# Kernel tuning notes

Measured on AMD Instinct MI355X. Metric: run time of the kernel, lower is better.

## Reference

```python
import jax, jax.numpy as jnp
import numpy as np

N_NODES = 100000
N_EDGES = 600000
D_FEAT = 128          # node embedding dim; in_channels = 2*D_FEAT = 256
HIDDEN = [128, 64]
OUT = 2


def setup_inputs() -> dict:
    key = jax.random.key(0)
    ks = jax.random.split(key, 8)
    enc = jax.random.normal(ks[0], (N_NODES, D_FEAT), dtype=jnp.float32)
    edge_index = jax.random.randint(ks[1], (2, N_EDGES), 0, N_NODES, dtype=jnp.int64)
    d_in = 2 * D_FEAT
    # Linear params, (in, out) layout; kaiming-ish scale
    W1 = jax.random.normal(ks[2], (d_in, HIDDEN[0]), dtype=jnp.float32) / np.sqrt(d_in)
    b1 = jnp.zeros((HIDDEN[0],), dtype=jnp.float32)
    W2 = jax.random.normal(ks[3], (HIDDEN[0], HIDDEN[1]), dtype=jnp.float32) / np.sqrt(HIDDEN[0])
    b2 = jnp.zeros((HIDDEN[1],), dtype=jnp.float32)
    W3 = jax.random.normal(ks[4], (HIDDEN[1], OUT), dtype=jnp.float32) / np.sqrt(HIDDEN[1])
    b3 = jnp.zeros((OUT,), dtype=jnp.float32)
    return {"encoder_output": enc, "edge_index": edge_index,
            "W1": W1, "b1": b1, "W2": W2, "b2": b2, "W3": W3, "b3": b3}


def reference(encoder_output, edge_index, W1, b1, W2, b2, W3, b3):
    row, col = edge_index[0], edge_index[1]
    # gather endpoint embeddings and concat -> [E, 2*D]
    x = jnp.concatenate([encoder_output[row], encoder_output[col]], axis=-1)
    h = jax.nn.relu(x @ W1 + b1)          # [E, 128]
    h = jax.nn.relu(h @ W2 + b2)          # [E, 64]
    logits = h @ W3 + b3                  # [E, 2]
    return jax.nn.log_softmax(logits, axis=-1)
```

## Files before the change

kernel.cpp:

```cpp
#include <hip/hip_runtime.h>
#include <hip/hip_fp16.h>

#define E_TOTAL  600000
#define N_NODES  100000
#define DFEAT    128
#define TPB_TILES 2
#define EPT      128
#define EPB      (EPT * TPB_TILES)
#define NB       ((E_TOTAL + EPB - 1) / EPB)

typedef __attribute__((ext_vector_type(8))) short     short8;
typedef __attribute__((ext_vector_type(8))) _Float16  half8;
typedef __attribute__((ext_vector_type(4))) float     f32x4;

static __device__ __forceinline__ unsigned short f2h(float f) {
    _Float16 h = (_Float16)f;
    return __builtin_bit_cast(unsigned short, h);
}

static __device__ __forceinline__ f32x4 mfma_f16(short8 a, short8 b, f32x4 c) {
    return __builtin_amdgcn_mfma_f32_16x16x32_f16(
        __builtin_bit_cast(half8, a), __builtin_bit_cast(half8, b), c, 0, 0, 0);
}

static __device__ __forceinline__ short8 h8_add_relu(short8 a, short8 b) {
    half8 s = __builtin_bit_cast(half8, a) + __builtin_bit_cast(half8, b);
    half8 z = {};
    s = __builtin_elementwise_max(s, z);
    return __builtin_bit_cast(short8, s);
}

__global__ void prep_w_fast(const float* __restrict__ W1, const float* __restrict__ W2,
                            unsigned short* __restrict__ w1abt, unsigned short* __restrict__ w2t) {
    int i = blockIdx.x * blockDim.x + threadIdx.x;
    if (i < 256 * 128) {
        int c = i >> 7, k = i & 127;
        w1abt[i] = f2h(W1[(k + (c & 128)) * 128 + (c & 127)]);
    } else {
        int j = i - 256 * 128;
        if (j < 64 * 128) {
            int c = j >> 7, k = j & 127;
            w2t[j] = f2h(W2[k * 64 + c]);
        }
    }
}

__global__ __launch_bounds__(256, 4) void build_pq(
        const float* __restrict__ enc, const float* __restrict__ b1,
        const unsigned short* __restrict__ w1abt, unsigned short* __restrict__ PQ)
{
    __shared__ unsigned short sX[64 * 128];

    const int tid = threadIdx.x, lane = tid & 63, w = tid >> 6;
    const int acol = lane & 15, g = lane >> 4;
    const int n0 = blockIdx.x * 64;

    {
        int r = tid >> 2, q = tid & 3;
        int n = n0 + r; if (n >= N_NODES) n = N_NODES - 1;
        const float* src = enc + (size_t)n * DFEAT + q * 32;
#pragma unroll
        for (int i = 0; i < 4; ++i) {
            float4 v0 = *reinterpret_cast<const float4*>(src + i * 8);
            float4 v1 = *reinterpret_cast<const float4*>(src + i * 8 + 4);
            short8 pv;
            pv[0] = (short)f2h(v0.x); pv[1] = (short)f2h(v0.y);
            pv[2] = (short)f2h(v0.z); pv[3] = (short)f2h(v0.w);
            pv[4] = (short)f2h(v1.x); pv[5] = (short)f2h(v1.y);
            pv[6] = (short)f2h(v1.z); pv[7] = (short)f2h(v1.w);
            int chunk = (q * 4 + i) ^ (r & 7);
            *reinterpret_cast<short8*>(&sX[r * 128 + chunk * 8]) = pv;
        }
    }
    float b1v[4];
#pragma unroll
    for (int ni = 0; ni < 4; ++ni) {
        int c = w * 64 + ni * 16 + acol;
        b1v[ni] = (c < 128) ? b1[c] : 0.f;
    }
    __syncthreads();

    f32x4 acc[4][4];
#pragma unroll
    for (int mi = 0; mi < 4; ++mi)
#pragma unroll
        for (int ni = 0; ni < 4; ++ni)
            acc[mi][ni] = (f32x4){0.f, 0.f, 0.f, 0.f};

#pragma unroll
    for (int ks = 0; ks < 4; ++ks) {
        short8 a[4];
#pragma unroll
        for (int mi = 0; mi < 4; ++mi) {
            int r = mi * 16 + acol;
            a[mi] = *reinterpret_cast<const short8*>(&sX[r * 128 + (((ks * 4 + g) ^ (r & 7)) * 8)]);
        }
#pragma unroll
        for (int ni = 0; ni < 4; ++ni) {
            int c = w * 64 + ni * 16 + acol;
            short8 bf = *reinterpret_cast<const short8*>(w1abt + c * 128 + ks * 32 + g * 8);
#pragma unroll
            for (int mi = 0; mi < 4; ++mi)
                acc[mi][ni] = mfma_f16(a[mi], bf, acc[mi][ni]);
        }
    }

#pragma unroll
    for (int mi = 0; mi < 4; ++mi)
#pragma unroll
        for (int rr = 0; rr < 4; ++rr) {
            int n = n0 + mi * 16 + g * 4 + rr;
            if (n < N_NODES) {
                unsigned short* dst = PQ + (size_t)n * 256 + w * 64 + acol;
#pragma unroll
                for (int ni = 0; ni < 4; ++ni)
                    dst[ni * 16] = f2h(acc[mi][ni][rr] + b1v[ni]);
            }
        }
}

__global__ __launch_bounds__(512, 4) void edge_head(
        const unsigned short* __restrict__ PQ,
        const int* __restrict__ eidx,
        const unsigned short* __restrict__ w2t,
        const float* __restrict__ b2, const float* __restrict__ W3, const float* __restrict__ b3,
        float* __restrict__ out)
{
    __shared__ unsigned short sH1[128 * 128];
    __shared__ unsigned short sW2[64 * 128];
    __shared__ float sB2[64];
    __shared__ float sW3[128];

    const int tid = threadIdx.x, lane = tid & 63, w = tid >> 6;
    const int e16 = lane & 15, g = lane >> 4;
    const int le = tid >> 2, q = tid & 3;

    {
        int c = tid >> 3, s = tid & 7;
#pragma unroll
        for (int h = 0; h < 2; ++h) {
            int cs = s + h * 8;
            short8 v = *reinterpret_cast<const short8*>(w2t + c * 128 + cs * 8);
            *reinterpret_cast<short8*>(&sW2[c * 128 + ((cs ^ (c & 7)) * 8)]) = v;
        }
    }
    if (tid < 64)       sB2[tid] = b2[tid];
    else if (tid < 192) sW3[tid - 64] = W3[tid - 64];
    const float b3v0 = b3[0], b3v1 = b3[1];

    const int tile0 = blockIdx.x * TPB_TILES;
    short8 rp[4], rq[4];
    {
        int e = tile0 * EPT + le; if (e >= E_TOTAL) e = E_TOTAL - 1;
        int sn = eidx[e], dn = eidx[E_TOTAL + e];
        const unsigned short* ps = PQ + (size_t)sn * 256 + q * 32;
        const unsigned short* pd = PQ + (size_t)dn * 256 + 128 + q * 32;
#pragma unroll
        for (int i = 0; i < 4; ++i) {
            rp[i] = *reinterpret_cast<const short8*>(ps + i * 8);
            rq[i] = *reinterpret_cast<const short8*>(pd + i * 8);
        }
    }

    for (int tl = 0; tl < TPB_TILES; ++tl) {
        const int tile = tile0 + tl;

#pragma unroll
        for (int i = 0; i < 4; ++i) {
            short8 hv = h8_add_relu(rp[i], rq[i]);
            int chunk = (q * 4 + i) ^ (le & 7);
            *reinterpret_cast<short8*>(&sH1[le * 128 + chunk * 8]) = hv;
        }

        if (tl + 1 < TPB_TILES) {
            int e = (tile + 1) * EPT + le; if (e >= E_TOTAL) e = E_TOTAL - 1;
            int sn = eidx[e], dn = eidx[E_TOTAL + e];
            const unsigned short* ps = PQ + (size_t)sn * 256 + q * 32;
            const unsigned short* pd = PQ + (size_t)dn * 256 + 128 + q * 32;
#pragma unroll
            for (int i = 0; i < 4; ++i) {
                rp[i] = *reinterpret_cast<const short8*>(ps + i * 8);
                rq[i] = *reinterpret_cast<const short8*>(pd + i * 8);
            }
        }
        __syncthreads();

        const int hrow = w * 16 + e16;
        f32x4 acc[4];
#pragma unroll
        for (int t = 0; t < 4; ++t) acc[t] = (f32x4){0.f, 0.f, 0.f, 0.f};
#pragma unroll
        for (int ks = 0; ks < 4; ++ks) {
            short8 hb = *reinterpret_cast<const short8*>(
                &sH1[hrow * 128 + (((ks * 4 + g) ^ (hrow & 7)) * 8)]);
#pragma unroll
            for (int t = 0; t < 4; ++t) {
                int ch = t * 16 + e16;
                short8 av = *reinterpret_cast<const short8*>(
                    &sW2[ch * 128 + (((ks * 4 + g) ^ (ch & 7)) * 8)]);
                acc[t] = mfma_f16(av, hb, acc[t]);
            }
        }

        float lg0 = 0.f, lg1 = 0.f;
#pragma unroll
        for (int t = 0; t < 4; ++t) {
            int c0 = t * 16 + g * 4;
            float4 bb  = *reinterpret_cast<const float4*>(&sB2[c0]);
            float4 w30 = *reinterpret_cast<const float4*>(&sW3[c0 * 2]);
            float4 w31 = *reinterpret_cast<const float4*>(&sW3[c0 * 2 + 4]);
            float h0 = fmaxf(acc[t][0] + bb.x, 0.f);
            float h1 = fmaxf(acc[t][1] + bb.y, 0.f);
            float h2 = fmaxf(acc[t][2] + bb.z, 0.f);
            float h3 = fmaxf(acc[t][3] + bb.w, 0.f);
            lg0 = fmaf(h0, w30.x, lg0); lg1 = fmaf(h0, w30.y, lg1);
            lg0 = fmaf(h1, w30.z, lg0); lg1 = fmaf(h1, w30.w, lg1);
            lg0 = fmaf(h2, w31.x, lg0); lg1 = fmaf(h2, w31.y, lg1);
            lg0 = fmaf(h3, w31.z, lg0); lg1 = fmaf(h3, w31.w, lg1);
        }
        lg0 += __shfl_xor(lg0, 16, 64); lg1 += __shfl_xor(lg1, 16, 64);
        lg0 += __shfl_xor(lg0, 32, 64); lg1 += __shfl_xor(lg1, 32, 64);

        int ge = tile * EPT + hrow;
        if (g == 0 && ge < E_TOTAL) {
            float v0 = lg0 + b3v0, v1 = lg1 + b3v1;
            float m = fmaxf(v0, v1);
            float lse = m + __logf(__expf(v0 - m) + __expf(v1 - m));
            *reinterpret_cast<float2*>(out + (size_t)ge * 2) = make_float2(v0 - lse, v1 - lse);
        }
        __syncthreads();
    }
}


extern "C" void kernel_launch(void* const* d_in, const int* in_sizes, int n_in,
                              void* d_out, int out_size, void* d_ws, size_t ws_size,
                              hipStream_t stream) {
    const float* enc = (const float*)d_in[0];
    const int*   eidx = (const int*)d_in[1];
    const float* W1 = (const float*)d_in[2];
    const float* b1 = (const float*)d_in[3];
    const float* W2 = (const float*)d_in[4];
    const float* b2 = (const float*)d_in[5];
    const float* W3 = (const float*)d_in[6];
    const float* b3 = (const float*)d_in[7];
    float* out = (float*)d_out;

    unsigned short* PQ    = (unsigned short*)d_ws;
    unsigned short* w1abt = PQ + (size_t)N_NODES * 256;
    unsigned short* w2t   = w1abt + 256 * 128;

    prep_w_fast<<<160, 256, 0, stream>>>(W1, W2, w1abt, w2t);
    build_pq<<<(N_NODES + 63) / 64, 256, 0, stream>>>(enc, b1, w1abt, PQ);
    edge_head<<<NB, 512, 0, stream>>>(PQ, eidx, w2t, b2, W3, b3, out);
}
```

Before: 86.61 us.

## Gather edge features directly into MFMA registers per wave, drop LDS staging

Each wave now processes its own 16-edge steps, loading the P/Q node rows straight into the MFMA operand layout instead of staging the H1 tile through shared memory. The next step's rows and the indices two steps ahead are prefetched in registers, and the per-tile block barriers are removed. Block size and LDS footprint shrink, trading fewer total blocks for less synchronisation and shared-memory traffic.

```diff
diff --git a/kernel.cpp b/kernel.cpp
--- a/kernel.cpp
+++ b/kernel.cpp
@@ -4,9 +4,9 @@
 #define E_TOTAL  600000
 #define N_NODES  100000
 #define DFEAT    128
-#define TPB_TILES 2
-#define EPT      128
-#define EPB      (EPT * TPB_TILES)
+#define STEPS    8
+#define WPB      4
+#define EPB      (WPB * STEPS * 16)
 #define NB       ((E_TOTAL + EPB - 1) / EPB)
 
 typedef __attribute__((ext_vector_type(8))) short     short8;
@@ -119,27 +119,25 @@
         }
 }
 
-__global__ __launch_bounds__(512, 4) void edge_head(
+__global__ __launch_bounds__(256, 4) void edge_head(
         const unsigned short* __restrict__ PQ,
         const int* __restrict__ eidx,
         const unsigned short* __restrict__ w2t,
         const float* __restrict__ b2, const float* __restrict__ W3, const float* __restrict__ b3,
         float* __restrict__ out)
 {
-    __shared__ unsigned short sH1[128 * 128];
     __shared__ unsigned short sW2[64 * 128];
     __shared__ float sB2[64];
     __shared__ float sW3[128];
 
     const int tid = threadIdx.x, lane = tid & 63, w = tid >> 6;
     const int e16 = lane & 15, g = lane >> 4;
-    const int le = tid >> 2, q = tid & 3;
-
-    {
-        int c = tid >> 3, s = tid & 7;
-#pragma unroll
-        for (int h = 0; h < 2; ++h) {
-            int cs = s + h * 8;
+
+    {
+        int c = tid >> 2, qq = tid & 3;
+#pragma unroll
+        for (int h = 0; h < 4; ++h) {
+            int cs = qq * 4 + h;
             short8 v = *reinterpret_cast<const short8*>(w2t + c * 128 + cs * 8);
             *reinterpret_cast<short8*>(&sW2[c * 128 + ((cs ^ (c & 7)) * 8)]) = v;
         }
@@ -147,58 +145,58 @@
     if (tid < 64)       sB2[tid] = b2[tid];
     else if (tid < 192) sW3[tid - 64] = W3[tid - 64];
     const float b3v0 = b3[0], b3v1 = b3[1];
-
-    const int tile0 = blockIdx.x * TPB_TILES;
-    short8 rp[4], rq[4];
-    {
-        int e = tile0 * EPT + le; if (e >= E_TOTAL) e = E_TOTAL - 1;
-        int sn = eidx[e], dn = eidx[E_TOTAL + e];
-        const unsigned short* ps = PQ + (size_t)sn * 256 + q * 32;
-        const unsigned short* pd = PQ + (size_t)dn * 256 + 128 + q * 32;
-#pragma unroll
-        for (int i = 0; i < 4; ++i) {
-            rp[i] = *reinterpret_cast<const short8*>(ps + i * 8);
-            rq[i] = *reinterpret_cast<const short8*>(pd + i * 8);
-        }
-    }
-
-    for (int tl = 0; tl < TPB_TILES; ++tl) {
-        const int tile = tile0 + tl;
-
-#pragma unroll
-        for (int i = 0; i < 4; ++i) {
-            short8 hv = h8_add_relu(rp[i], rq[i]);
-            int chunk = (q * 4 + i) ^ (le & 7);
-            *reinterpret_cast<short8*>(&sH1[le * 128 + chunk * 8]) = hv;
-        }
-
-        if (tl + 1 < TPB_TILES) {
-            int e = (tile + 1) * EPT + le; if (e >= E_TOTAL) e = E_TOTAL - 1;
-            int sn = eidx[e], dn = eidx[E_TOTAL + e];
-            const unsigned short* ps = PQ + (size_t)sn * 256 + q * 32;
-            const unsigned short* pd = PQ + (size_t)dn * 256 + 128 + q * 32;
-#pragma unroll
-            for (int i = 0; i < 4; ++i) {
-                rp[i] = *reinterpret_cast<const short8*>(ps + i * 8);
-                rq[i] = *reinterpret_cast<const short8*>(pd + i * 8);
+    __syncthreads();
+
+    const int ebase = (blockIdx.x * WPB + w) * (STEPS * 16) + e16;
+
+    short8 p[4], q[4];
+    {
+        int E = ebase; if (E >= E_TOTAL) E = E_TOTAL - 1;
+        int sn = eidx[E], dn = eidx[E_TOTAL + E];
+        const unsigned short* ps = PQ + (size_t)sn * 256 + g * 8;
+        const unsigned short* pd = PQ + (size_t)dn * 256 + 128 + g * 8;
+#pragma unroll
+        for (int ks = 0; ks < 4; ++ks) {
+            p[ks] = *reinterpret_cast<const short8*>(ps + ks * 32);
+            q[ks] = *reinterpret_cast<const short8*>(pd + ks * 32);
+        }
+    }
+    int snN, dnN;
+    {
+        int E = ebase + 16; if (E >= E_TOTAL) E = E_TOTAL - 1;
+        snN = eidx[E]; dnN = eidx[E_TOTAL + E];
+    }
+
+    for (int s = 0; s < STEPS; ++s) {
+        short8 hb[4];
+#pragma unroll
+        for (int ks = 0; ks < 4; ++ks) hb[ks] = h8_add_relu(p[ks], q[ks]);
+
+        if (s + 1 < STEPS) {
+            const unsigned short* ps = PQ + (size_t)snN * 256 + g * 8;
+            const unsigned short* pd = PQ + (size_t)dnN * 256 + 128 + g * 8;
+#pragma unroll
+            for (int ks = 0; ks < 4; ++ks) {
+                p[ks] = *reinterpret_cast<const short8*>(ps + ks * 32);
+                q[ks] = *reinterpret_cast<const short8*>(pd + ks * 32);
             }
         }
-        __syncthreads();
-
-        const int hrow = w * 16 + e16;
+        if (s + 2 < STEPS) {
+            int E = ebase + (s + 2) * 16; if (E >= E_TOTAL) E = E_TOTAL - 1;
+            snN = eidx[E]; dnN = eidx[E_TOTAL + E];
+        }
+
         f32x4 acc[4];
 #pragma unroll
         for (int t = 0; t < 4; ++t) acc[t] = (f32x4){0.f, 0.f, 0.f, 0.f};
 #pragma unroll
         for (int ks = 0; ks < 4; ++ks) {
-            short8 hb = *reinterpret_cast<const short8*>(
-                &sH1[hrow * 128 + (((ks * 4 + g) ^ (hrow & 7)) * 8)]);
 #pragma unroll
             for (int t = 0; t < 4; ++t) {
                 int ch = t * 16 + e16;
                 short8 av = *reinterpret_cast<const short8*>(
                     &sW2[ch * 128 + (((ks * 4 + g) ^ (ch & 7)) * 8)]);
-                acc[t] = mfma_f16(av, hb, acc[t]);
+                acc[t] = mfma_f16(av, hb[ks], acc[t]);
             }
         }
 
@@ -221,14 +219,13 @@
         lg0 += __shfl_xor(lg0, 16, 64); lg1 += __shfl_xor(lg1, 16, 64);
         lg0 += __shfl_xor(lg0, 32, 64); lg1 += __shfl_xor(lg1, 32, 64);
 
-        int ge = tile * EPT + hrow;
+        int ge = ebase + s * 16;
         if (g == 0 && ge < E_TOTAL) {
             float v0 = lg0 + b3v0, v1 = lg1 + b3v1;
             float m = fmaxf(v0, v1);
             float lse = m + __logf(__expf(v0 - m) + __expf(v1 - m));
             *reinterpret_cast<float2*>(out + (size_t)ge * 2) = make_float2(v0 - lse, v1 - lse);
         }
-        __syncthreads();
     }
 }
 
@@ -252,5 +249,5 @@
 
     prep_w_fast<<<160, 256, 0, stream>>>(W1, W2, w1abt, w2t);
     build_pq<<<(N_NODES + 63) / 64, 256, 0, stream>>>(enc, b1, w1abt, PQ);
-    edge_head<<<NB, 512, 0, stream>>>(PQ, eidx, w2t, b2, W3, b3, out);
-}
+    edge_head<<<NB, 256, 0, stream>>>(PQ, eidx, w2t, b2, W3, b3, out);
+}
```

Result: slower. 154.9 us (+78.9%).
